# Optimization experiments

Measured on AMD Instinct MI355X. Metric: run time of the kernel, lower is better.

The kernel has to match this reference:

```python
import jax, jax.numpy as jnp
import numpy as np

D_MODEL = 1024
N_HEADS = 16
B, S = 4, 2048
SCALE = float(np.sqrt(D_MODEL))  # NOTE: source scales by sqrt(d_key)=sqrt(full dim), not sqrt(head dim)


def setup_inputs() -> dict:
    key = jax.random.key(0)
    ks = jax.random.split(key, 6)
    inv = 1.0 / np.sqrt(D_MODEL)
    return {
        "query": jax.random.normal(ks[0], (B, S, D_MODEL), dtype=jnp.float32),
        "key": jax.random.normal(ks[1], (B, S, D_MODEL), dtype=jnp.float32),
        "value": jax.random.normal(ks[2], (B, S, D_MODEL), dtype=jnp.float32),
        # torch Linear weights: [out_features, in_features], y = x @ W.T
        "wq": jax.random.uniform(ks[3], (D_MODEL, D_MODEL), jnp.float32, -inv, inv),
        "wk": jax.random.uniform(ks[4], (D_MODEL, D_MODEL), jnp.float32, -inv, inv),
        "wv": jax.random.uniform(ks[5], (D_MODEL, D_MODEL), jnp.float32, -inv, inv),
    }


def reference(query, key, value, wq, wk, wv):
    dh = D_MODEL // N_HEADS
    b, sq, _ = query.shape
    sk = key.shape[1]
    # projections (bias=False): x @ W.T
    q = (query @ wq.T).reshape(b, sq, N_HEADS, dh)
    k = (key @ wk.T).reshape(b, sk, N_HEADS, dh)
    v = (value @ wv.T).reshape(b, sk, N_HEADS, dh)
    # per-head scores; chunk(-1) == contiguous head split, same as reshape
    scores = jnp.einsum("bqhd,bkhd->bhqk", q, k) / SCALE
    probs = jax.nn.softmax(scores, axis=-1)
    out = jnp.einsum("bhqk,bkhd->bqhd", probs, v)
    return out.reshape(b, sq, D_MODEL)
```

## Files before the change

kernel.cpp:

```cpp
#include <hip/hip_runtime.h>
#include <hip/hip_bf16.h>
#include <stdint.h>

typedef __bf16 bf16;
typedef __attribute__((ext_vector_type(8))) __bf16 bf16x8;
typedef __attribute__((ext_vector_type(4))) __bf16 bf16x4;
typedef __attribute__((ext_vector_type(4))) float f32x4;

#define S_LEN 2048
#define DMODEL 1024
#define NH 16
#define BATCH 4

#define NX 8388608u
#define NW 1048576u
#define WC_OFF (3u * NX)
#define PP_OFF (WC_OFF + 3u * NW)

static __device__ __forceinline__ void gload_lds16(const void* g, void* l) {
  __builtin_amdgcn_global_load_lds(
      (const __attribute__((address_space(1))) void*)(g),
      (__attribute__((address_space(3))) void*)(l), 16, 0, 0);
}

static __device__ __forceinline__ void wait_lds() {
  asm volatile("s_waitcnt lgkmcnt(0)" ::: "memory");
}

struct CvtArgs {
  const float* s[6];
  bf16* d[6];
  int n[6];
};

__global__ __launch_bounds__(256) void cvt_f32_bf16(CvtArgs a) {
  const int ai = blockIdx.y;
  const float* __restrict__ s = a.s[ai];
  bf16* __restrict__ d = a.d[ai];
  const int n = a.n[ai];
  const int i = (blockIdx.x * 256 + threadIdx.x) * 8;
  if (i >= n) return;
  const float4* sp = reinterpret_cast<const float4*>(s + i);
  float4 x = sp[0];
  float4 y = sp[1];
  bf16x8 o;
  o[0] = (bf16)x.x; o[1] = (bf16)x.y; o[2] = (bf16)x.z; o[3] = (bf16)x.w;
  o[4] = (bf16)y.x; o[5] = (bf16)y.y; o[6] = (bf16)y.z; o[7] = (bf16)y.w;
  *reinterpret_cast<bf16x8*>(d + i) = o;
}

__global__ __launch_bounds__(256, 3) void proj_gemm(const bf16* __restrict__ Xc,
                                                    const bf16* __restrict__ Wc,
                                                    bf16* __restrict__ Yp) {
  const int z = blockIdx.z;
  const bf16* __restrict__ X = Xc + (size_t)z * NX;
  const bf16* __restrict__ W = Wc + (size_t)z * NW;
  bf16* __restrict__ Y = Yp + (size_t)z * NX;

  __shared__ bf16 ldsA[2][128 * 32];
  __shared__ bf16 ldsB[2][128 * 32];

  const int tid = threadIdx.x;
  const int lane = tid & 63;
  const int w = tid >> 6;
  const int wr = w >> 1, wc = w & 1;
  const int r16 = lane & 15, g4 = lane >> 4;
  const int m0 = blockIdx.x * 128, n0 = blockIdx.y * 128;

  f32x4 acc[4][4];
#pragma unroll
  for (int mi = 0; mi < 4; mi++)
#pragma unroll
    for (int ni = 0; ni < 4; ni++) acc[mi][ni] = (f32x4){0.f, 0.f, 0.f, 0.f};

  const int rowa = tid >> 2;
  const int cola = (tid & 3) * 8;

  auto stage = [&](int buf, int k0) {
    gload_lds16(X + (size_t)(m0 + rowa) * DMODEL + k0 + cola, &ldsA[buf][tid * 8]);
    gload_lds16(X + (size_t)(m0 + 64 + rowa) * DMODEL + k0 + cola,
                &ldsA[buf][2048 + tid * 8]);
    gload_lds16(W + (size_t)(n0 + rowa) * DMODEL + k0 + cola, &ldsB[buf][tid * 8]);
    gload_lds16(W + (size_t)(n0 + 64 + rowa) * DMODEL + k0 + cola,
                &ldsB[buf][2048 + tid * 8]);
  };

  stage(0, 0);
  __syncthreads();
  int cur = 0;

  for (int k0 = 0; k0 < DMODEL; k0 += 32) {
    if (k0 + 32 < DMODEL) stage(cur ^ 1, k0 + 32);

    bf16x8 af[4], bfr[4];
#pragma unroll
    for (int mi = 0; mi < 4; mi++)
      af[mi] = *reinterpret_cast<const bf16x8*>(
          &ldsA[cur][(wr * 64 + mi * 16 + r16) * 32 + g4 * 8]);
#pragma unroll
    for (int ni = 0; ni < 4; ni++)
      bfr[ni] = *reinterpret_cast<const bf16x8*>(
          &ldsB[cur][(wc * 64 + ni * 16 + r16) * 32 + g4 * 8]);
    __builtin_amdgcn_s_setprio(1);
#pragma unroll
    for (int mi = 0; mi < 4; mi++)
#pragma unroll
      for (int ni = 0; ni < 4; ni++)
        acc[mi][ni] = __builtin_amdgcn_mfma_f32_16x16x32_bf16(
            af[mi], bfr[ni], acc[mi][ni], 0, 0, 0);
    __builtin_amdgcn_s_setprio(0);
    __syncthreads();
    cur ^= 1;
  }

  float* shf = reinterpret_cast<float*>(&ldsA[0][0]) + w * 1024;
#pragma unroll
  for (int mi = 0; mi < 4; mi++) {
#pragma unroll
    for (int ni = 0; ni < 4; ni++)
#pragma unroll
      for (int i = 0; i < 4; i++) {
        const int rl = g4 * 4 + i;
        const int cl = ni * 16 + r16;
        shf[rl * 64 + ((cl + 4 * rl) & 63)] = acc[mi][ni][i];
      }
    wait_lds();
#pragma unroll
    for (int cc = 0; cc < 4; cc++) {
      const int row = g4 + cc * 4;
      const int c0 = r16 * 4;
      const f32x4 vv = *reinterpret_cast<const f32x4*>(
          &shf[row * 64 + ((c0 + 4 * row) & 63)]);
      bf16x4 o;
      o[0] = (bf16)vv[0]; o[1] = (bf16)vv[1]; o[2] = (bf16)vv[2]; o[3] = (bf16)vv[3];
      *reinterpret_cast<bf16x4*>(
          Y + (size_t)(m0 + wr * 64 + mi * 16 + row) * DMODEL + n0 + wc * 64 + c0) = o;
    }
    wait_lds();
  }
}

__global__ __launch_bounds__(256, 3) void attn_kernel(const bf16* __restrict__ Qp,
                                                      const bf16* __restrict__ Kp,
                                                      const bf16* __restrict__ Vp,
                                                      float* __restrict__ Out) {
  __shared__ bf16 ldsK[2][64 * 64];
  __shared__ bf16 ldsVt[2][64 * 64];
  __shared__ bf16 ldsP[4][32 * 64];

  const int tid = threadIdx.x;
  const int lane = tid & 63;
  const int w = tid >> 6;
  const int r16 = lane & 15, g4 = lane >> 4;
  const int b = blockIdx.z, h = blockIdx.y;
  const int q0 = blockIdx.x * 128 + w * 32;

  bf16x8 qf[2][2];
#pragma unroll
  for (int qi = 0; qi < 2; qi++)
#pragma unroll
    for (int kk = 0; kk < 2; kk++)
      qf[qi][kk] = *reinterpret_cast<const bf16x8*>(
          Qp + (size_t)(b * S_LEN + q0 + qi * 16 + r16) * DMODEL + h * 64 +
          kk * 32 + g4 * 8);

  f32x4 oacc[2][4];
#pragma unroll
  for (int mi = 0; mi < 2; mi++)
#pragma unroll
    for (int nd = 0; nd < 4; nd++) oacc[mi][nd] = (f32x4){0.f, 0.f, 0.f, 0.f};

  float mrun[2] = {-1e30f, -1e30f};
  float lrun[2] = {0.f, 0.f};
  const float C2 = 0.04508422002778011f;

  const int srow = tid >> 3;
  const int scol = (tid & 7) * 8;
  const int kswz = (srow & 7) * 8;

  auto stageK = [&](int buf, int kv0) {
    gload_lds16(Kp + (size_t)(b * S_LEN + kv0 + srow) * DMODEL + h * 64 + (scol ^ kswz),
                &ldsK[buf][tid * 8]);
    gload_lds16(Kp + (size_t)(b * S_LEN + kv0 + 32 + srow) * DMODEL + h * 64 + (scol ^ kswz),
                &ldsK[buf][2048 + tid * 8]);
  };
  bf16x8 vpre0, vpre1;
  auto loadV = [&](int kv0) {
    vpre0 = *reinterpret_cast<const bf16x8*>(
        Vp + (size_t)(b * S_LEN + kv0 + srow) * DMODEL + h * 64 + scol);
    vpre1 = *reinterpret_cast<const bf16x8*>(
        Vp + (size_t)(b * S_LEN + kv0 + 32 + srow) * DMODEL + h * 64 + scol);
  };
  auto writeV = [&](int buf) {
#pragma unroll
    for (int j = 0; j < 8; j++) {
      const int d = scol + j;
      const int vsw = (((scol >> 3) ^ j) & 7) * 8;
      ldsVt[buf][d * 64 + (srow ^ vsw)] = vpre0[j];
      ldsVt[buf][d * 64 + ((srow + 32) ^ vsw)] = vpre1[j];
    }
  };

  stageK(0, 0);
  loadV(0);
  writeV(0);
  __syncthreads();
  int cur = 0;

  constexpr int NT = S_LEN / 64;
  for (int it = 0; it < NT; it++) {
    const bool pf = (it + 1 < NT);
    if (pf) {
      stageK(cur ^ 1, (it + 1) * 64);
      loadV((it + 1) * 64);
    }

    f32x4 sacc[4][2];
#pragma unroll
    for (int kvi = 0; kvi < 4; kvi++)
#pragma unroll
      for (int qi = 0; qi < 2; qi++) sacc[kvi][qi] = (f32x4){0.f, 0.f, 0.f, 0.f};
#pragma unroll
    for (int kk = 0; kk < 2; kk++) {
      bf16x8 kf[4];
#pragma unroll
      for (int kvi = 0; kvi < 4; kvi++) {
        const int kvr = kvi * 16 + r16;
        const int c = (kk * 32 + g4 * 8) ^ ((r16 & 7) * 8);
        kf[kvi] = *reinterpret_cast<const bf16x8*>(&ldsK[cur][kvr * 64 + c]);
      }
      __builtin_amdgcn_s_setprio(1);
#pragma unroll
      for (int kvi = 0; kvi < 4; kvi++)
#pragma unroll
        for (int qi = 0; qi < 2; qi++)
          sacc[kvi][qi] = __builtin_amdgcn_mfma_f32_16x16x32_bf16(
              kf[kvi], qf[qi][kk], sacc[kvi][qi], 0, 0, 0);
      __builtin_amdgcn_s_setprio(0);
    }

#pragma unroll
    for (int qi = 0; qi < 2; qi++) {
      float tmax = -1e30f;
#pragma unroll
      for (int kvi = 0; kvi < 4; kvi++)
#pragma unroll
        for (int i = 0; i < 4; i++) tmax = fmaxf(tmax, sacc[kvi][qi][i]);
      tmax = fmaxf(tmax, __shfl_xor(tmax, 16, 64));
      tmax = fmaxf(tmax, __shfl_xor(tmax, 32, 64));
      const float tm2 = tmax * C2;
      const bool resc = !__all(tm2 <= mrun[qi] + 11.0f);
      float mnew = mrun[qi], corr = 1.f;
      if (resc) {
        mnew = fmaxf(mrun[qi], tm2);
        corr = exp2f(mrun[qi] - mnew);
      }
      float psum = 0.f;
      const int q = qi * 16 + r16;
#pragma unroll
      for (int kvi = 0; kvi < 4; kvi++) {
        float p0 = exp2f(fmaf(sacc[kvi][qi][0], C2, -mnew));
        float p1 = exp2f(fmaf(sacc[kvi][qi][1], C2, -mnew));
        float p2 = exp2f(fmaf(sacc[kvi][qi][2], C2, -mnew));
        float p3 = exp2f(fmaf(sacc[kvi][qi][3], C2, -mnew));
        psum += (p0 + p1) + (p2 + p3);
        const int kvbase = (kvi * 16 + g4 * 4) ^ ((q & 7) * 8);
        bf16x4 pk;
        pk[0] = (bf16)p0; pk[1] = (bf16)p1; pk[2] = (bf16)p2; pk[3] = (bf16)p3;
        *reinterpret_cast<bf16x4*>(&ldsP[w][q * 64 + kvbase]) = pk;
      }
      psum += __shfl_xor(psum, 16, 64);
      psum += __shfl_xor(psum, 32, 64);
      if (resc) {
        lrun[qi] = lrun[qi] * corr + psum;
        mrun[qi] = mnew;
#pragma unroll
        for (int i = 0; i < 4; i++) {
          const float corr_r = __shfl(corr, g4 * 4 + i, 64);
#pragma unroll
          for (int nd = 0; nd < 4; nd++) oacc[qi][nd][i] *= corr_r;
        }
      } else {
        lrun[qi] += psum;
      }
    }

#pragma unroll
    for (int kk = 0; kk < 2; kk++) {
      bf16x8 pfg[2], vf[4];
#pragma unroll
      for (int mi = 0; mi < 2; mi++) {
        const int q = mi * 16 + r16;
        const int c = (kk * 32 + g4 * 8) ^ ((q & 7) * 8);
        pfg[mi] = *reinterpret_cast<const bf16x8*>(&ldsP[w][q * 64 + c]);
      }
#pragma unroll
      for (int nd = 0; nd < 4; nd++) {
        const int d = nd * 16 + r16;
        const int c = (kk * 32 + g4 * 8) ^ ((((d >> 3) ^ d) & 7) * 8);
        vf[nd] = *reinterpret_cast<const bf16x8*>(&ldsVt[cur][d * 64 + c]);
      }
      __builtin_amdgcn_s_setprio(1);
#pragma unroll
      for (int mi = 0; mi < 2; mi++)
#pragma unroll
        for (int nd = 0; nd < 4; nd++)
          oacc[mi][nd] = __builtin_amdgcn_mfma_f32_16x16x32_bf16(
              pfg[mi], vf[nd], oacc[mi][nd], 0, 0, 0);
      __builtin_amdgcn_s_setprio(0);
    }

    if (pf) writeV(cur ^ 1);
    __syncthreads();
    cur ^= 1;
  }

#pragma unroll
  for (int mi = 0; mi < 2; mi++)
#pragma unroll
    for (int i = 0; i < 4; i++) {
      const float lr = __shfl(lrun[mi], g4 * 4 + i, 64);
      const float inv_l = 1.0f / lr;
      const int q = q0 + mi * 16 + g4 * 4 + i;
#pragma unroll
      for (int nd = 0; nd < 4; nd++)
        Out[(size_t)(b * S_LEN + q) * DMODEL + h * 64 + nd * 16 + r16] =
            oacc[mi][nd][i] * inv_l;
    }
}

extern "C" void kernel_launch(void* const* d_in, const int* in_sizes, int n_in,
                              void* d_out, int out_size, void* d_ws, size_t ws_size,
                              hipStream_t stream) {
  const float* q = (const float*)d_in[0];
  const float* k = (const float*)d_in[1];
  const float* v = (const float*)d_in[2];
  const float* wq = (const float*)d_in[3];
  const float* wk = (const float*)d_in[4];
  const float* wv = (const float*)d_in[5];
  bf16* ws = (bf16*)d_ws;
  bf16* Xc = ws;
  bf16* Wc = ws + WC_OFF;
  bf16* Pp = ws + PP_OFF;
  float* out = (float*)d_out;

  CvtArgs ca;
  ca.s[0] = q;  ca.s[1] = k;  ca.s[2] = v;
  ca.s[3] = wq; ca.s[4] = wk; ca.s[5] = wv;
  ca.d[0] = Xc;          ca.d[1] = Xc + NX;     ca.d[2] = Xc + 2 * NX;
  ca.d[3] = Wc;          ca.d[4] = Wc + NW;     ca.d[5] = Wc + 2 * NW;
  ca.n[0] = ca.n[1] = ca.n[2] = (int)NX;
  ca.n[3] = ca.n[4] = ca.n[5] = (int)NW;
  cvt_f32_bf16<<<dim3(4096, 6, 1), dim3(256), 0, stream>>>(ca);

  proj_gemm<<<dim3(64, 8, 3), dim3(256), 0, stream>>>(Xc, Wc, Pp);

  attn_kernel<<<dim3(S_LEN / 128, NH, BATCH), dim3(256), 0, stream>>>(
      Pp, Pp + NX, Pp + 2 * NX, out);
}
```

Baseline: 353.5 us.

## Switch attention to 32x32x16 MFMA and keep P in registers via permlane swap

Rewrites the attention inner loop around 32x32x16 bf16 MFMA tiles, so each lane owns one query row's scores. Softmax probabilities go straight from the S accumulator into the PV MFMA A-operand using v_cvt_pk_bf16_f32 and v_permlane32_swap, which removes the ldsP shared-memory round trip. The max and sum reductions need fewer cross-lane shuffles, and occupancy is raised to 4 blocks per CU because LDS use drops. The risks are higher register pressure from the f32x16 accumulators under the tighter launch bound, and a more intricate operand layout that has to match the MFMA lane mapping exactly.

```diff
diff --git a/kernel.cpp b/kernel.cpp
--- a/kernel.cpp
+++ b/kernel.cpp
@@ -6,6 +6,8 @@
 typedef __attribute__((ext_vector_type(8))) __bf16 bf16x8;
 typedef __attribute__((ext_vector_type(4))) __bf16 bf16x4;
 typedef __attribute__((ext_vector_type(4))) float f32x4;
+typedef __attribute__((ext_vector_type(16))) float f32x16;
+typedef __attribute__((ext_vector_type(4))) uint32_t u32x4;
 
 #define S_LEN 2048
 #define DMODEL 1024
@@ -25,6 +27,15 @@
 
 static __device__ __forceinline__ void wait_lds() {
   asm volatile("s_waitcnt lgkmcnt(0)" ::: "memory");
+}
+
+static __device__ __forceinline__ uint32_t cvtpk(float lo, float hi) {
+  uint32_t r;
+  asm("v_cvt_pk_bf16_f32 %0, %1, %2" : "=v"(r) : "v"(lo), "v"(hi));
+  return r;
+}
+static __device__ __forceinline__ void pl32swap(uint32_t& a, uint32_t& b) {
+  asm volatile("v_permlane32_swap_b32 %0, %1" : "+v"(a), "+v"(b));
 }
 
 struct CvtArgs {
@@ -140,38 +151,32 @@
   }
 }
 
-__global__ __launch_bounds__(256, 3) void attn_kernel(const bf16* __restrict__ Qp,
+__global__ __launch_bounds__(256, 4) void attn_kernel(const bf16* __restrict__ Qp,
                                                       const bf16* __restrict__ Kp,
                                                       const bf16* __restrict__ Vp,
                                                       float* __restrict__ Out) {
   __shared__ bf16 ldsK[2][64 * 64];
   __shared__ bf16 ldsVt[2][64 * 64];
-  __shared__ bf16 ldsP[4][32 * 64];
 
   const int tid = threadIdx.x;
   const int lane = tid & 63;
   const int w = tid >> 6;
-  const int r16 = lane & 15, g4 = lane >> 4;
+  const int l31 = lane & 31, hi = lane >> 5;
   const int b = blockIdx.z, h = blockIdx.y;
   const int q0 = blockIdx.x * 128 + w * 32;
 
-  bf16x8 qf[2][2];
-#pragma unroll
-  for (int qi = 0; qi < 2; qi++)
-#pragma unroll
-    for (int kk = 0; kk < 2; kk++)
-      qf[qi][kk] = *reinterpret_cast<const bf16x8*>(
-          Qp + (size_t)(b * S_LEN + q0 + qi * 16 + r16) * DMODEL + h * 64 +
-          kk * 32 + g4 * 8);
-
-  f32x4 oacc[2][4];
-#pragma unroll
-  for (int mi = 0; mi < 2; mi++)
-#pragma unroll
-    for (int nd = 0; nd < 4; nd++) oacc[mi][nd] = (f32x4){0.f, 0.f, 0.f, 0.f};
-
-  float mrun[2] = {-1e30f, -1e30f};
-  float lrun[2] = {0.f, 0.f};
+  bf16x8 qf[4];
+#pragma unroll
+  for (int s = 0; s < 4; s++)
+    qf[s] = *reinterpret_cast<const bf16x8*>(
+        Qp + (size_t)(b * S_LEN + q0 + l31) * DMODEL + h * 64 + s * 16 + hi * 8);
+
+  f32x16 oacc[2];
+  oacc[0] = (f32x16)0.f;
+  oacc[1] = (f32x16)0.f;
+
+  float mrun = -1e30f;
+  float lrun = 0.f;
   const float C2 = 0.04508422002778011f;
 
   const int srow = tid >> 3;
@@ -215,100 +220,96 @@
       loadV((it + 1) * 64);
     }
 
-    f32x4 sacc[4][2];
-#pragma unroll
-    for (int kvi = 0; kvi < 4; kvi++)
-#pragma unroll
-      for (int qi = 0; qi < 2; qi++) sacc[kvi][qi] = (f32x4){0.f, 0.f, 0.f, 0.f};
-#pragma unroll
-    for (int kk = 0; kk < 2; kk++) {
-      bf16x8 kf[4];
-#pragma unroll
-      for (int kvi = 0; kvi < 4; kvi++) {
-        const int kvr = kvi * 16 + r16;
-        const int c = (kk * 32 + g4 * 8) ^ ((r16 & 7) * 8);
-        kf[kvi] = *reinterpret_cast<const bf16x8*>(&ldsK[cur][kvr * 64 + c]);
-      }
-      __builtin_amdgcn_s_setprio(1);
-#pragma unroll
-      for (int kvi = 0; kvi < 4; kvi++)
-#pragma unroll
-        for (int qi = 0; qi < 2; qi++)
-          sacc[kvi][qi] = __builtin_amdgcn_mfma_f32_16x16x32_bf16(
-              kf[kvi], qf[qi][kk], sacc[kvi][qi], 0, 0, 0);
-      __builtin_amdgcn_s_setprio(0);
-    }
-
-#pragma unroll
-    for (int qi = 0; qi < 2; qi++) {
-      float tmax = -1e30f;
-#pragma unroll
-      for (int kvi = 0; kvi < 4; kvi++)
-#pragma unroll
-        for (int i = 0; i < 4; i++) tmax = fmaxf(tmax, sacc[kvi][qi][i]);
-      tmax = fmaxf(tmax, __shfl_xor(tmax, 16, 64));
-      tmax = fmaxf(tmax, __shfl_xor(tmax, 32, 64));
-      const float tm2 = tmax * C2;
-      const bool resc = !__all(tm2 <= mrun[qi] + 11.0f);
-      float mnew = mrun[qi], corr = 1.f;
-      if (resc) {
-        mnew = fmaxf(mrun[qi], tm2);
-        corr = exp2f(mrun[qi] - mnew);
-      }
-      float psum = 0.f;
-      const int q = qi * 16 + r16;
-#pragma unroll
-      for (int kvi = 0; kvi < 4; kvi++) {
-        float p0 = exp2f(fmaf(sacc[kvi][qi][0], C2, -mnew));
-        float p1 = exp2f(fmaf(sacc[kvi][qi][1], C2, -mnew));
-        float p2 = exp2f(fmaf(sacc[kvi][qi][2], C2, -mnew));
-        float p3 = exp2f(fmaf(sacc[kvi][qi][3], C2, -mnew));
-        psum += (p0 + p1) + (p2 + p3);
-        const int kvbase = (kvi * 16 + g4 * 4) ^ ((q & 7) * 8);
-        bf16x4 pk;
-        pk[0] = (bf16)p0; pk[1] = (bf16)p1; pk[2] = (bf16)p2; pk[3] = (bf16)p3;
-        *reinterpret_cast<bf16x4*>(&ldsP[w][q * 64 + kvbase]) = pk;
-      }
-      psum += __shfl_xor(psum, 16, 64);
-      psum += __shfl_xor(psum, 32, 64);
-      if (resc) {
-        lrun[qi] = lrun[qi] * corr + psum;
-        mrun[qi] = mnew;
-#pragma unroll
-        for (int i = 0; i < 4; i++) {
-          const float corr_r = __shfl(corr, g4 * 4 + i, 64);
-#pragma unroll
-          for (int nd = 0; nd < 4; nd++) oacc[qi][nd][i] *= corr_r;
+    f32x16 sacc[2];
+    sacc[0] = (f32x16)0.f;
+    sacc[1] = (f32x16)0.f;
+#pragma unroll
+    for (int kvh = 0; kvh < 2; kvh++) {
+#pragma unroll
+      for (int s = 0; s < 4; s++) {
+        const int kv = kvh * 32 + l31;
+        const bf16x8 kf = *reinterpret_cast<const bf16x8*>(
+            &ldsK[cur][kv * 64 + ((s * 16 + hi * 8) ^ ((l31 & 7) * 8))]);
+        __builtin_amdgcn_s_setprio(1);
+        sacc[kvh] = __builtin_amdgcn_mfma_f32_32x32x16_bf16(kf, qf[s], sacc[kvh], 0, 0, 0);
+        __builtin_amdgcn_s_setprio(0);
+      }
+    }
+
+    float tmax = -1e30f;
+#pragma unroll
+    for (int kvh = 0; kvh < 2; kvh++)
+#pragma unroll
+      for (int r = 0; r < 16; r++) tmax = fmaxf(tmax, sacc[kvh][r]);
+    tmax = fmaxf(tmax, __shfl_xor(tmax, 32, 64));
+    const float tm2 = tmax * C2;
+    const bool resc = !__all(tm2 <= mrun + 11.0f);
+    float corr = 1.f;
+    if (resc) {
+      const float mnew = fmaxf(mrun, tm2);
+      corr = exp2f(mrun - mnew);
+      mrun = mnew;
+    }
+    float psum = 0.f;
+#pragma unroll
+    for (int kvh = 0; kvh < 2; kvh++)
+#pragma unroll
+      for (int r = 0; r < 16; r++) {
+        const float p = exp2f(fmaf(sacc[kvh][r], C2, -mrun));
+        sacc[kvh][r] = p;
+        psum += p;
+      }
+    psum += __shfl_xor(psum, 32, 64);
+    if (resc) {
+      lrun = lrun * corr + psum;
+#pragma unroll
+      for (int r = 0; r < 16; r++) {
+        const int qrow = (r & 3) + 8 * (r >> 2) + 4 * hi;
+        const float cr = __int_as_float(
+            __builtin_amdgcn_ds_bpermute(qrow * 4, __float_as_int(corr)));
+        oacc[0][r] *= cr;
+        oacc[1][r] *= cr;
+      }
+    } else {
+      lrun += psum;
+    }
+
+    union U { u32x4 u; bf16x8 v; };
+    U pa[2][2];
+#pragma unroll
+    for (int kvh = 0; kvh < 2; kvh++) {
+      uint32_t a0 = cvtpk(sacc[kvh][0], sacc[kvh][1]);
+      uint32_t b0 = cvtpk(sacc[kvh][4], sacc[kvh][5]);
+      pl32swap(a0, b0);
+      uint32_t a1 = cvtpk(sacc[kvh][2], sacc[kvh][3]);
+      uint32_t b1 = cvtpk(sacc[kvh][6], sacc[kvh][7]);
+      pl32swap(a1, b1);
+      pa[kvh][0].u = (u32x4){a0, a1, b0, b1};
+      uint32_t a2 = cvtpk(sacc[kvh][8], sacc[kvh][9]);
+      uint32_t b2 = cvtpk(sacc[kvh][12], sacc[kvh][13]);
+      pl32swap(a2, b2);
+      uint32_t a3 = cvtpk(sacc[kvh][10], sacc[kvh][11]);
+      uint32_t b3 = cvtpk(sacc[kvh][14], sacc[kvh][15]);
+      pl32swap(a3, b3);
+      pa[kvh][1].u = (u32x4){a2, a3, b2, b3};
+    }
+
+#pragma unroll
+    for (int kvh = 0; kvh < 2; kvh++)
+#pragma unroll
+      for (int sh = 0; sh < 2; sh++) {
+        const int kvb = kvh * 32 + sh * 16 + hi * 8;
+#pragma unroll
+        for (int db = 0; db < 2; db++) {
+          const int d = db * 32 + l31;
+          const bf16x8 vf = *reinterpret_cast<const bf16x8*>(
+              &ldsVt[cur][d * 64 + (kvb ^ ((((d >> 3) ^ d) & 7) * 8))]);
+          __builtin_amdgcn_s_setprio(1);
+          oacc[db] = __builtin_amdgcn_mfma_f32_32x32x16_bf16(pa[kvh][sh].v, vf,
+                                                             oacc[db], 0, 0, 0);
+          __builtin_amdgcn_s_setprio(0);
         }
-      } else {
-        lrun[qi] += psum;
-      }
-    }
-
-#pragma unroll
-    for (int kk = 0; kk < 2; kk++) {
-      bf16x8 pfg[2], vf[4];
-#pragma unroll
-      for (int mi = 0; mi < 2; mi++) {
-        const int q = mi * 16 + r16;
-        const int c = (kk * 32 + g4 * 8) ^ ((q & 7) * 8);
-        pfg[mi] = *reinterpret_cast<const bf16x8*>(&ldsP[w][q * 64 + c]);
-      }
-#pragma unroll
-      for (int nd = 0; nd < 4; nd++) {
-        const int d = nd * 16 + r16;
-        const int c = (kk * 32 + g4 * 8) ^ ((((d >> 3) ^ d) & 7) * 8);
-        vf[nd] = *reinterpret_cast<const bf16x8*>(&ldsVt[cur][d * 64 + c]);
-      }
-      __builtin_amdgcn_s_setprio(1);
-#pragma unroll
-      for (int mi = 0; mi < 2; mi++)
-#pragma unroll
-        for (int nd = 0; nd < 4; nd++)
-          oacc[mi][nd] = __builtin_amdgcn_mfma_f32_16x16x32_bf16(
-              pfg[mi], vf[nd], oacc[mi][nd], 0, 0, 0);
-      __builtin_amdgcn_s_setprio(0);
-    }
+      }
 
     if (pf) writeV(cur ^ 1);
     __syncthreads();
@@ -316,17 +317,15 @@
   }
 
 #pragma unroll
-  for (int mi = 0; mi < 2; mi++)
-#pragma unroll
-    for (int i = 0; i < 4; i++) {
-      const float lr = __shfl(lrun[mi], g4 * 4 + i, 64);
-      const float inv_l = 1.0f / lr;
-      const int q = q0 + mi * 16 + g4 * 4 + i;
-#pragma unroll
-      for (int nd = 0; nd < 4; nd++)
-        Out[(size_t)(b * S_LEN + q) * DMODEL + h * 64 + nd * 16 + r16] =
-            oacc[mi][nd][i] * inv_l;
-    }
+  for (int r = 0; r < 16; r++) {
+    const int qrow = (r & 3) + 8 * (r >> 2) + 4 * hi;
+    const float lr = __int_as_float(
+        __builtin_amdgcn_ds_bpermute(qrow * 4, __float_as_int(lrun)));
+    const float inv_l = 1.0f / lr;
+    float* op = Out + (size_t)(b * S_LEN + q0 + qrow) * DMODEL + h * 64 + l31;
+    op[0] = oacc[0][r] * inv_l;
+    op[32] = oacc[1][r] * inv_l;
+  }
 }
 
 extern "C" void kernel_launch(void* const* d_in, const int* in_sizes, int n_in,
```

New measurement: 421.6 us. +19.3%, slower.
